# Kernel optimization log

Hardware: AMD Instinct MI355X
Metric: run time of the kernel (lower is better)

## Reference

```python
import jax, jax.numpy as jnp
import numpy as np

DIM = 1024
NUM_HEADS = 16
HEAD_DIM = DIM // NUM_HEADS
ROPE_THETA = 10000.0
SCALE = HEAD_DIM ** -0.5


def _apply_rope(x, cos, sin):
    # x: [B, H, S, head_dim]; cos/sin: [S, head_dim//2] (broadcast over B, H)
    x_even = x[..., 0::2]
    x_odd = x[..., 1::2]
    rot_even = x_even * cos - x_odd * sin
    rot_odd = x_even * sin + x_odd * cos
    # interleave back: stack on last axis then flatten, matching torch .stack(-1).flatten(-2)
    return jnp.stack([rot_even, rot_odd], axis=-1).reshape(x.shape)


def setup_inputs() -> dict:
    key = jax.random.key(0)
    k0, k1, k2 = jax.random.split(key, 3)
    B, S = 2, 2048
    x = jax.random.normal(k0, (B, S, DIM), dtype=jnp.float32)
    # small_init: std = sqrt(2 / (5*dim))
    qkv_w = jax.random.normal(k1, (3 * DIM, DIM), dtype=jnp.float32) * (2.0 / (5 * DIM)) ** 0.5
    qkv_b = jnp.zeros((3 * DIM,), dtype=jnp.float32)
    # wang_init: std = 2 / num_blocks / sqrt(dim) scaled
    out_w = jax.random.normal(k2, (DIM, DIM), dtype=jnp.float32) * (2.0 / DIM) ** 0.5 / 2.0
    out_b = jnp.zeros((DIM,), dtype=jnp.float32)
    return {"x": x, "qkv_w": qkv_w, "qkv_b": qkv_b, "out_w": out_w, "out_b": out_b, "window_size": 512}


def reference(x, qkv_w, qkv_b, out_w, out_b, window_size):
    B, S, D = x.shape
    qkv = x @ qkv_w.T + qkv_b                          # [B, S, 3D]
    qkv = qkv.reshape(B, S, 3, NUM_HEADS, HEAD_DIM).transpose(2, 0, 3, 1, 4)
    q, k, v = qkv[0], qkv[1], qkv[2]                   # each [B, H, S, hd]

    pos = jnp.arange(S, dtype=jnp.float32)
    inv_freq = 1.0 / (ROPE_THETA ** (jnp.arange(0, HEAD_DIM, 2, dtype=jnp.float32) / HEAD_DIM))
    freqs = pos[:, None] * inv_freq                    # [S, hd//2]
    cos, sin = jnp.cos(freqs), jnp.sin(freqs)
    q = _apply_rope(q, cos, sin)
    k = _apply_rope(k, cos, sin)

    scores = jnp.einsum('bhqd,bhkd->bhqk', q, k) * SCALE
    i = jnp.arange(S)
    mask = (i[:, None] >= i[None, :]) & ((i[:, None] - i[None, :]) < window_size)  # causal sliding window
    scores = jnp.where(mask, scores, -jnp.inf)
    attn = jax.nn.softmax(scores, axis=-1)
    out = jnp.einsum('bhqk,bhkd->bhqd', attn, v)       # [B, H, S, hd]
    out = out.transpose(0, 2, 1, 3).reshape(B, S, D)
    return out @ out_w.T + out_b
```

## Files before the change

kernel.cpp:

```cpp
#include <hip/hip_runtime.h>
#include <hip/hip_bf16.h>
#include <cstdint>
#include <cstddef>

using bf16x8 = __attribute__((ext_vector_type(8))) short;
using f32x4  = __attribute__((ext_vector_type(4))) float;

#define MFMA16(a, b, c) __builtin_amdgcn_mfma_f32_16x16x32_bf16((a), (b), (c), 0, 0, 0)

__device__ __forceinline__ unsigned short f2bf(float f) {
    unsigned int u = __float_as_uint(f);
    u += 0x7fffu + ((u >> 16) & 1u);
    return (unsigned short)(u >> 16);
}
__device__ __forceinline__ uint32_t pack2bf(float a, float b) {
    __hip_bfloat162 h = __float22bfloat162_rn(float2{a, b});
    return *(uint32_t*)&h;
}
__device__ __forceinline__ float bflo(uint32_t p) { return __uint_as_float(p << 16); }
__device__ __forceinline__ float bfhi(uint32_t p) { return __uint_as_float(p & 0xffff0000u); }

__device__ __forceinline__ void gload_lds16(const void* g, void* l) {
    __builtin_amdgcn_global_load_lds(
        (const __attribute__((address_space(1))) void*)g,
        (__attribute__((address_space(3))) void*)l, 16, 0, 0);
}

#define S_LEN 2048
#define NHEAD 16
#define HDIM  64
#define DIM   1024
#define WIN   512
#define BATCH 2
#define MROWS 4096

__global__ void prep(float* __restrict__ cosT, float* __restrict__ sinT,
                     const float* __restrict__ x, unsigned short* __restrict__ xb,
                     const float* __restrict__ qw, unsigned short* __restrict__ qwb,
                     const float* __restrict__ ow, unsigned short* __restrict__ owb) {
    int t = blockIdx.x * 256 + threadIdx.x;
    if (t < 65536) {
        int s = t >> 5, f = t & 31;
        float invf = powf(10000.0f, -(float)f / 32.0f);
        float ang = (float)s * invf;
        cosT[t] = cosf(ang);
        sinT[t] = sinf(ang);
        return;
    }
    int u = t - 65536;
    const float* src;
    unsigned short* dst;
    int i;
    if (u < 1048576)        { src = x;  dst = xb;  i = u * 4; }
    else if (u < 1835008)   { src = qw; dst = qwb; i = (u - 1048576) * 4; }
    else                    { src = ow; dst = owb; i = (u - 1835008) * 4; }
    float4 v = *(const float4*)(src + i);
    ushort4 o;
    o.x = f2bf(v.x); o.y = f2bf(v.y); o.z = f2bf(v.z); o.w = f2bf(v.w);
    *(ushort4*)(dst + i) = o;
}

template <int OUT_BF16>
__global__ __launch_bounds__(256) void gemm_nt(const unsigned short* __restrict__ A,
                                               const unsigned short* __restrict__ Bw,
                                               const float* __restrict__ bias,
                                               void* __restrict__ Cout, int N, int K) {
    __shared__ short As[128 * 32];
    __shared__ short Bs[128 * 32];
    const int tid = threadIdx.x;
    const int lane = tid & 63, w = tid >> 6;
    const int wr = w >> 1, wc = w & 1, lm = lane & 15, lg = lane >> 4;
    const int row0 = blockIdx.y * 128, col0 = blockIdx.x * 128;

    f32x4 acc[4][4];
#pragma unroll
    for (int m = 0; m < 4; ++m)
#pragma unroll
        for (int n = 0; n < 4; ++n) acc[m][n] = (f32x4){0.f, 0.f, 0.f, 0.f};

    const size_t ldb = (size_t)K * 2;
    for (int kt = 0; kt < K; kt += 32) {
#pragma unroll
        for (int i = 0; i < 2; ++i) {
            int c = tid + 256 * i;
            int r = c >> 2, kc = c & 3;
            gload_lds16((const char*)A  + (size_t)(row0 + r) * ldb + (size_t)kt * 2 + kc * 16, &As[c * 8]);
            gload_lds16((const char*)Bw + (size_t)(col0 + r) * ldb + (size_t)kt * 2 + kc * 16, &Bs[c * 8]);
        }
        __syncthreads();
        bf16x8 af[4], bfr[4];
#pragma unroll
        for (int m = 0; m < 4; ++m) af[m]  = *(const bf16x8*)&As[(wr * 64 + m * 16 + lm) * 32 + lg * 8];
#pragma unroll
        for (int n = 0; n < 4; ++n) bfr[n] = *(const bf16x8*)&Bs[(wc * 64 + n * 16 + lm) * 32 + lg * 8];
#pragma unroll
        for (int m = 0; m < 4; ++m)
#pragma unroll
            for (int n = 0; n < 4; ++n) acc[m][n] = MFMA16(af[m], bfr[n], acc[m][n]);
        __syncthreads();
    }

#pragma unroll
    for (int m = 0; m < 4; ++m) {
        int row = row0 + wr * 64 + m * 16 + lg * 4;
#pragma unroll
        for (int n = 0; n < 4; ++n) {
            int col = col0 + wc * 64 + n * 16 + lm;
            float bv = bias[col];
#pragma unroll
            for (int r = 0; r < 4; ++r) {
                float v = acc[m][n][r] + bv;
                if (OUT_BF16)
                    ((unsigned short*)Cout)[(size_t)(row + r) * N + col] = f2bf(v);
                else
                    ((float*)Cout)[(size_t)(row + r) * N + col] = v;
            }
        }
    }
}

__global__ void rope_pack(const unsigned short* __restrict__ qkvb,
                          const float* __restrict__ cosT, const float* __restrict__ sinT,
                          unsigned short* __restrict__ qb, unsigned short* __restrict__ kb) {
    int t = blockIdx.x * 256 + threadIdx.x;
    int p = t & 511, m = t >> 9;
    int h = p >> 5, f = p & 31;
    int s = m & (S_LEN - 1), b = m >> 11;
    float c = cosT[s * 32 + f], sn = sinT[s * 32 + f];
    const float SC = 0.125f;

    uint32_t qp = *(const uint32_t*)&qkvb[m * 3072 + h * 64 + 2 * f];
    float qe = bflo(qp), qo = bfhi(qp);
    float re = (qe * c - qo * sn) * SC, ro = (qe * sn + qo * c) * SC;
    *(uint32_t*)&qb[((b * NHEAD + h) * S_LEN + s) * 64 + 2 * f] =
        (uint32_t)f2bf(re) | ((uint32_t)f2bf(ro) << 16);

    uint32_t kp = *(const uint32_t*)&qkvb[m * 3072 + 1024 + h * 64 + 2 * f];
    float ke = bflo(kp), ko = bfhi(kp);
    float rke = ke * c - ko * sn, rko = ke * sn + ko * c;
    *(uint32_t*)&kb[((b * NHEAD + h) * S_LEN + s) * 64 + 2 * f] =
        (uint32_t)f2bf(rke) | ((uint32_t)f2bf(rko) << 16);
}

__global__ __launch_bounds__(256) void v_transpose(const unsigned short* __restrict__ qkvb,
                                                   unsigned short* __restrict__ vt) {
    int st = blockIdx.x, bh = blockIdx.y;
    int h = bh & 15, b = bh >> 4;
    __shared__ unsigned short tile[64][72];
    int tid = threadIdx.x;
#pragma unroll
    for (int i = 0; i < 2; ++i) {
        int c = tid + 256 * i;
        int r = c >> 3, col = (c & 7) * 8;
        int m = b * S_LEN + st * 64 + r;
        *(bf16x8*)&tile[r][col] = *(const bf16x8*)&qkvb[m * 3072 + 2048 + h * 64 + col];
    }
    __syncthreads();
#pragma unroll
    for (int i = 0; i < 2; ++i) {
        int c = tid + 256 * i;
        int d = c >> 3, scol = (c & 7) * 8;
        unsigned short tmp[8];
#pragma unroll
        for (int j = 0; j < 8; ++j) tmp[j] = tile[scol + j][d];
        *(bf16x8*)&vt[(size_t)bh * 64 * S_LEN + (size_t)d * S_LEN + st * 64 + scol] = *(bf16x8*)tmp;
    }
}

__global__ __launch_bounds__(256) void attn(const unsigned short* __restrict__ qb,
                                            const unsigned short* __restrict__ kb,
                                            const unsigned short* __restrict__ vt,
                                            unsigned short* __restrict__ ao) {
    const int p = blockIdx.x;
    const int L = (p & 7) * 128 + (p >> 3);
    const int qblk = L & 31, bh = L >> 5;
    const int b = bh >> 4, h = bh & 15;
    const int tid = threadIdx.x, w = tid >> 6, lane = tid & 63;
    const int lm = lane & 15, lg = lane >> 4;
    const unsigned short* Qb = qb + (size_t)bh * S_LEN * 64;
    const unsigned short* Kb = kb + (size_t)bh * S_LEN * 64;
    const unsigned short* Vt = vt + (size_t)bh * 64 * S_LEN;
    const int q0 = qblk * 64 + w * 16;

    __shared__ short Ks[2][64 * 64];
    __shared__ short Vs[2][64 * 64];
    __shared__ short Plds[4][16 * 64];
    short* Pw = Plds[w];

    bf16x8 aq0 = *(const bf16x8*)&Qb[(q0 + lm) * 64 + lg * 8];
    bf16x8 aq1 = *(const bf16x8*)&Qb[(q0 + lm) * 64 + lg * 8 + 32];

    f32x4 o[4];
#pragma unroll
    for (int n = 0; n < 4; ++n) o[n] = (f32x4){0.f, 0.f, 0.f, 0.f};
    float lsum = 0.f;

    const int qq = q0 + lm;
    const int t0 = qblk >= 8 ? qblk - 8 : 0;

    auto stage = [&](int kt, int buf) {
#pragma unroll
        for (int i = 0; i < 2; ++i) {
            int c = tid + 256 * i;
            int r = c >> 3, g = (c & 7) ^ (r & 7);
            gload_lds16(Kb + (size_t)(kt * 64 + r) * 64 + g * 8, &Ks[buf][c * 8]);
            gload_lds16(Vt + (size_t)r * S_LEN + kt * 64 + g * 8, &Vs[buf][c * 8]);
        }
    };

    stage(t0, 0);
    __syncthreads();
    int cur = 0;
    for (int kt = t0; kt <= qblk; ++kt) {
        if (kt < qblk) stage(kt + 1, cur ^ 1);
        const int kbase = kt * 64;
        const int sw = lm & 7;
        f32x4 sT[4];
#pragma unroll
        for (int n = 0; n < 4; ++n) {
            int rl = n * 16 + lm;
            bf16x8 bk0 = *(const bf16x8*)&Ks[cur][rl * 64 + ((lg ^ sw) << 3)];
            bf16x8 bk1 = *(const bf16x8*)&Ks[cur][rl * 64 + (((lg + 4) ^ sw) << 3)];
            f32x4 z = (f32x4){0.f, 0.f, 0.f, 0.f};
            z = MFMA16(bk0, aq0, z);
            sT[n] = MFMA16(bk1, aq1, z);
        }
#pragma unroll
        for (int n = 0; n < 4; ++n) {
            int kk0 = kbase + n * 16 + lg * 4;
#pragma unroll
            for (int r = 0; r < 4; ++r) {
                int d = qq - (kk0 + r);
                float sv = ((unsigned)d < (unsigned)WIN) ? sT[n][r] : -1e30f;
                float pv = __expf(sv);
                sT[n][r] = pv;
                lsum += pv;
            }
            uint2 pk;
            pk.x = pack2bf(sT[n][0], sT[n][1]);
            pk.y = pack2bf(sT[n][2], sT[n][3]);
            *(uint2*)&Pw[lm * 64 + ((((2 * n + (lg >> 1)) ^ sw) << 3) + ((lg & 1) << 2))] = pk;
        }
        bf16x8 ap0 = *(const bf16x8*)&Pw[lm * 64 + ((lg ^ sw) << 3)];
        bf16x8 ap1 = *(const bf16x8*)&Pw[lm * 64 + (((lg + 4) ^ sw) << 3)];
#pragma unroll
        for (int n = 0; n < 4; ++n) {
            int rl = n * 16 + lm;
            bf16x8 bv0 = *(const bf16x8*)&Vs[cur][rl * 64 + ((lg ^ sw) << 3)];
            bf16x8 bv1 = *(const bf16x8*)&Vs[cur][rl * 64 + (((lg + 4) ^ sw) << 3)];
            o[n] = MFMA16(ap0, bv0, o[n]);
            o[n] = MFMA16(ap1, bv1, o[n]);
        }
        __syncthreads();
        cur ^= 1;
    }
    lsum += __shfl_xor(lsum, 16, 64);
    lsum += __shfl_xor(lsum, 32, 64);
    float linv = 1.f / lsum;
    float lrow[4];
#pragma unroll
    for (int r = 0; r < 4; ++r) lrow[r] = __shfl(linv, lg * 4 + r, 64);
#pragma unroll
    for (int n = 0; n < 4; ++n)
#pragma unroll
        for (int r = 0; r < 4; ++r) {
            int row = b * S_LEN + q0 + lg * 4 + r;
            int col = h * 64 + n * 16 + lm;
            ao[(size_t)row * DIM + col] = f2bf(o[n][r] * lrow[r]);
        }
}

extern "C" void kernel_launch(void* const* d_in, const int* in_sizes, int n_in,
                              void* d_out, int out_size, void* d_ws, size_t ws_size,
                              hipStream_t stream) {
    const float* x      = (const float*)d_in[0];
    const float* qkv_w  = (const float*)d_in[1];
    const float* qkv_b  = (const float*)d_in[2];
    const float* out_w  = (const float*)d_in[3];
    const float* out_b  = (const float*)d_in[4];
    (void)in_sizes; (void)n_in; (void)out_size; (void)ws_size;

    char* ws = (char*)d_ws;
    float*          cosT = (float*)(ws + 0);
    float*          sinT = (float*)(ws + (256 << 10));
    unsigned short* xb   = (unsigned short*)(ws + (512 << 10));
    unsigned short* wqb  = (unsigned short*)(ws + 8912896);
    unsigned short* owb  = (unsigned short*)(ws + 15204352);
    unsigned short* qkvb = (unsigned short*)(ws + 17301504);
    unsigned short* qbuf = (unsigned short*)(ws + 42467328);
    unsigned short* kbuf = (unsigned short*)(ws + 50855936);
    unsigned short* vtb  = (unsigned short*)(ws + 59244544);
    unsigned short* aob  = (unsigned short*)(ws + 67633152);

    prep<<<8448, 256, 0, stream>>>(cosT, sinT, x, xb, qkv_w, wqb, out_w, owb);

    gemm_nt<1><<<dim3(24, 32), 256, 0, stream>>>(xb, wqb, qkv_b, qkvb, 3 * DIM, DIM);

    rope_pack<<<8192, 256, 0, stream>>>(qkvb, cosT, sinT, qbuf, kbuf);
    v_transpose<<<dim3(32, 32), 256, 0, stream>>>(qkvb, vtb);

    attn<<<1024, 256, 0, stream>>>(qbuf, kbuf, vtb, aob);

    gemm_nt<0><<<dim3(8, 32), 256, 0, stream>>>(aob, owb, out_b, d_out, DIM, DIM);
}
```

Baseline: 111.4 us.

## Fuse RoPE and V transpose into QKV GEMM epilogue, double-buffer and swizzle GEMM LDS

The QKV projection GEMM now applies bias, RoPE and Q scaling in its epilogue and writes Q/K in head-major layout and V transposed, staging tiles through LDS. This removes the rope_pack and v_transpose kernels and the intermediate qkv buffer round trip. Both GEMMs also gain double-buffered LDS staging with one barrier per k-step and an XOR swizzle on LDS columns to cut bank conflicts. The epilogue adds extra barriers and LDS traffic, and the GEMMs hardcode K=1024.

```diff
diff --git a/kernel.cpp b/kernel.cpp
--- a/kernel.cpp
+++ b/kernel.cpp
@@ -16,6 +16,9 @@
 __device__ __forceinline__ uint32_t pack2bf(float a, float b) {
     __hip_bfloat162 h = __float22bfloat162_rn(float2{a, b});
     return *(uint32_t*)&h;
+}
+__device__ __forceinline__ float bf2f(short x) {
+    return __uint_as_float(((uint32_t)(unsigned short)x) << 16);
 }
 __device__ __forceinline__ float bflo(uint32_t p) { return __uint_as_float(p << 16); }
 __device__ __forceinline__ float bfhi(uint32_t p) { return __uint_as_float(p & 0xffff0000u); }
@@ -31,7 +34,6 @@
 #define HDIM  64
 #define DIM   1024
 #define WIN   512
-#define BATCH 2
 #define MROWS 4096
 
 __global__ void prep(float* __restrict__ cosT, float* __restrict__ sinT,
@@ -60,13 +62,145 @@
     *(ushort4*)(dst + i) = o;
 }
 
-template <int OUT_BF16>
-__global__ __launch_bounds__(256) void gemm_nt(const unsigned short* __restrict__ A,
-                                               const unsigned short* __restrict__ Bw,
-                                               const float* __restrict__ bias,
-                                               void* __restrict__ Cout, int N, int K) {
-    __shared__ short As[128 * 32];
-    __shared__ short Bs[128 * 32];
+
+__global__ __launch_bounds__(256) void gemm_qkv_fused(
+        const unsigned short* __restrict__ A,
+        const unsigned short* __restrict__ Bw,
+        const float* __restrict__ bias,
+        const float* __restrict__ cosT, const float* __restrict__ sinT,
+        unsigned short* __restrict__ qbuf,
+        unsigned short* __restrict__ kbuf,
+        unsigned short* __restrict__ vtb) {
+    __shared__ __align__(16) char smem_raw[32768];
+    const int tid = threadIdx.x;
+    const int lane = tid & 63, w = tid >> 6;
+    const int wr = w >> 1, wc = w & 1, lm = lane & 15, lg = lane >> 4;
+    const int bx = blockIdx.x, by = blockIdx.y;
+    const int row0 = by * 128, col0 = bx * 128;
+    const int plane = bx >> 3;
+    const int h0 = (bx & 7) * 2;
+    const int b = by >> 4, s_base = (by & 15) * 128;
+
+    f32x4 acc[4][4];
+#pragma unroll
+    for (int m = 0; m < 4; ++m)
+#pragma unroll
+        for (int n = 0; n < 4; ++n) acc[m][n] = (f32x4){0.f, 0.f, 0.f, 0.f};
+
+    auto As = [&](int buf) { return (short*)(smem_raw + buf * 16384); };
+    auto Bs = [&](int buf) { return (short*)(smem_raw + buf * 16384 + 8192); };
+
+    const size_t ldb = 2048;
+    auto stage = [&](int kt, int buf) {
+#pragma unroll
+        for (int i = 0; i < 2; ++i) {
+            int c = tid + 256 * i;
+            int r = c >> 2, gp = c & 3;
+            int gs = gp ^ ((r >> 1) & 3);
+            gload_lds16((const char*)A  + (size_t)(row0 + r) * ldb + (size_t)kt * 64 + gs * 16, As(buf) + c * 8);
+            gload_lds16((const char*)Bw + (size_t)(col0 + r) * ldb + (size_t)kt * 64 + gs * 16, Bs(buf) + c * 8);
+        }
+    };
+
+    stage(0, 0);
+    __syncthreads();
+    int cur = 0;
+    const int swz = (lm >> 1) & 3;
+    for (int kt = 0; kt < 32; ++kt) {
+        if (kt + 1 < 32) stage(kt + 1, cur ^ 1);
+        bf16x8 af[4], bfr[4];
+        const short* as = As(cur);
+        const short* bs = Bs(cur);
+#pragma unroll
+        for (int m = 0; m < 4; ++m) af[m]  = *(const bf16x8*)&as[(wr * 64 + m * 16 + lm) * 32 + ((lg ^ swz) << 3)];
+#pragma unroll
+        for (int n = 0; n < 4; ++n) bfr[n] = *(const bf16x8*)&bs[(wc * 64 + n * 16 + lm) * 32 + ((lg ^ swz) << 3)];
+#pragma unroll
+        for (int m = 0; m < 4; ++m)
+#pragma unroll
+            for (int n = 0; n < 4; ++n) acc[m][n] = MFMA16(af[m], bfr[n], acc[m][n]);
+        __syncthreads();
+        cur ^= 1;
+    }
+
+    unsigned short (*tile)[136] = (unsigned short(*)[136])smem_raw;
+    unsigned short (*tileT)[72] = (unsigned short(*)[72])smem_raw;
+    const int lane8 = tid & 7, idx = tid >> 3;
+
+#pragma unroll 1
+    for (int half = 0; half < 2; ++half) {
+        __syncthreads();
+        if (wr == half) {
+            if (plane < 2) {
+#pragma unroll
+                for (int m = 0; m < 4; ++m)
+#pragma unroll
+                    for (int n = 0; n < 4; ++n) {
+                        int colL = wc * 64 + n * 16 + lm;
+                        float bv = bias[col0 + colL];
+#pragma unroll
+                        for (int r = 0; r < 4; ++r)
+                            tile[m * 16 + lg * 4 + r][colL] = f2bf(acc[m][n][r] + bv);
+                    }
+            } else {
+#pragma unroll
+                for (int m = 0; m < 4; ++m)
+#pragma unroll
+                    for (int n = 0; n < 4; ++n) {
+                        int colL = wc * 64 + n * 16 + lm;
+                        float bv = bias[col0 + colL];
+                        uint2 pk;
+                        pk.x = pack2bf(acc[m][n][0] + bv, acc[m][n][1] + bv);
+                        pk.y = pack2bf(acc[m][n][2] + bv, acc[m][n][3] + bv);
+                        *(uint2*)&tileT[colL][m * 16 + lg * 4] = pk;
+                    }
+            }
+        }
+        __syncthreads();
+        if (plane < 2) {
+            unsigned short* dstp = (plane == 0) ? qbuf : kbuf;
+            const float qsc = (plane == 0) ? 0.125f : 1.0f;
+            int d0 = lane8 * 8;
+#pragma unroll
+            for (int j = 0; j < 2; ++j) {
+                int srow = idx + 32 * j;
+                int s = s_base + half * 64 + srow;
+                float4 c4 = *(const float4*)&cosT[s * 32 + (d0 >> 1)];
+                float4 s4 = *(const float4*)&sinT[s * 32 + (d0 >> 1)];
+#pragma unroll
+                for (int hh = 0; hh < 2; ++hh) {
+                    bf16x8 v = *(const bf16x8*)&tile[srow][hh * 64 + d0];
+                    float e0 = bf2f(v[0]), o0 = bf2f(v[1]);
+                    float e1 = bf2f(v[2]), o1 = bf2f(v[3]);
+                    float e2 = bf2f(v[4]), o2 = bf2f(v[5]);
+                    float e3 = bf2f(v[6]), o3 = bf2f(v[7]);
+                    uint4 pk;
+                    pk.x = pack2bf((e0 * c4.x - o0 * s4.x) * qsc, (e0 * s4.x + o0 * c4.x) * qsc);
+                    pk.y = pack2bf((e1 * c4.y - o1 * s4.y) * qsc, (e1 * s4.y + o1 * c4.y) * qsc);
+                    pk.z = pack2bf((e2 * c4.z - o2 * s4.z) * qsc, (e2 * s4.z + o2 * c4.z) * qsc);
+                    pk.w = pack2bf((e3 * c4.w - o3 * s4.w) * qsc, (e3 * s4.w + o3 * c4.w) * qsc);
+                    int h = h0 + hh;
+                    *(uint4*)&dstp[(((size_t)(b * NHEAD + h)) * S_LEN + s) * 64 + d0] = pk;
+                }
+            }
+        } else {
+#pragma unroll
+            for (int rr = 0; rr < 4; ++rr) {
+                int hd = rr * 32 + idx;
+                int hh = hd >> 6, d = hd & 63, h = h0 + hh;
+                bf16x8 v = *(const bf16x8*)&tileT[hd][lane8 * 8];
+                *(bf16x8*)&vtb[((size_t)(b * NHEAD + h) * 64 + d) * S_LEN +
+                               s_base + half * 64 + lane8 * 8] = v;
+            }
+        }
+    }
+}
+
+__global__ __launch_bounds__(256) void gemm_out(const unsigned short* __restrict__ A,
+                                                const unsigned short* __restrict__ Bw,
+                                                const float* __restrict__ bias,
+                                                float* __restrict__ Cout) {
+    __shared__ __align__(16) char smem_raw[32768];
     const int tid = threadIdx.x;
     const int lane = tid & 63, w = tid >> 6;
     const int wr = w >> 1, wc = w & 1, lm = lane & 15, lg = lane >> 4;
@@ -78,26 +212,40 @@
 #pragma unroll
         for (int n = 0; n < 4; ++n) acc[m][n] = (f32x4){0.f, 0.f, 0.f, 0.f};
 
-    const size_t ldb = (size_t)K * 2;
-    for (int kt = 0; kt < K; kt += 32) {
+    auto As = [&](int buf) { return (short*)(smem_raw + buf * 16384); };
+    auto Bs = [&](int buf) { return (short*)(smem_raw + buf * 16384 + 8192); };
+
+    const size_t ldb = 2048;
+    auto stage = [&](int kt, int buf) {
 #pragma unroll
         for (int i = 0; i < 2; ++i) {
             int c = tid + 256 * i;
-            int r = c >> 2, kc = c & 3;
-            gload_lds16((const char*)A  + (size_t)(row0 + r) * ldb + (size_t)kt * 2 + kc * 16, &As[c * 8]);
-            gload_lds16((const char*)Bw + (size_t)(col0 + r) * ldb + (size_t)kt * 2 + kc * 16, &Bs[c * 8]);
-        }
-        __syncthreads();
+            int r = c >> 2, gp = c & 3;
+            int gs = gp ^ ((r >> 1) & 3);
+            gload_lds16((const char*)A  + (size_t)(row0 + r) * ldb + (size_t)kt * 64 + gs * 16, As(buf) + c * 8);
+            gload_lds16((const char*)Bw + (size_t)(col0 + r) * ldb + (size_t)kt * 64 + gs * 16, Bs(buf) + c * 8);
+        }
+    };
+
+    stage(0, 0);
+    __syncthreads();
+    int cur = 0;
+    const int swz = (lm >> 1) & 3;
+    for (int kt = 0; kt < 32; ++kt) {
+        if (kt + 1 < 32) stage(kt + 1, cur ^ 1);
         bf16x8 af[4], bfr[4];
-#pragma unroll
-        for (int m = 0; m < 4; ++m) af[m]  = *(const bf16x8*)&As[(wr * 64 + m * 16 + lm) * 32 + lg * 8];
-#pragma unroll
-        for (int n = 0; n < 4; ++n) bfr[n] = *(const bf16x8*)&Bs[(wc * 64 + n * 16 + lm) * 32 + lg * 8];
+        const short* as = As(cur);
+        const short* bs = Bs(cur);
+#pragma unroll
+        for (int m = 0; m < 4; ++m) af[m]  = *(const bf16x8*)&as[(wr * 64 + m * 16 + lm) * 32 + ((lg ^ swz) << 3)];
+#pragma unroll
+        for (int n = 0; n < 4; ++n) bfr[n] = *(const bf16x8*)&bs[(wc * 64 + n * 16 + lm) * 32 + ((lg ^ swz) << 3)];
 #pragma unroll
         for (int m = 0; m < 4; ++m)
 #pragma unroll
             for (int n = 0; n < 4; ++n) acc[m][n] = MFMA16(af[m], bfr[n], acc[m][n]);
         __syncthreads();
+        cur ^= 1;
     }
 
 #pragma unroll
@@ -108,62 +256,9 @@
             int col = col0 + wc * 64 + n * 16 + lm;
             float bv = bias[col];
 #pragma unroll
-            for (int r = 0; r < 4; ++r) {
-                float v = acc[m][n][r] + bv;
-                if (OUT_BF16)
-                    ((unsigned short*)Cout)[(size_t)(row + r) * N + col] = f2bf(v);
-                else
-                    ((float*)Cout)[(size_t)(row + r) * N + col] = v;
-            }
-        }
-    }
-}
-
-__global__ void rope_pack(const unsigned short* __restrict__ qkvb,
-                          const float* __restrict__ cosT, const float* __restrict__ sinT,
-                          unsigned short* __restrict__ qb, unsigned short* __restrict__ kb) {
-    int t = blockIdx.x * 256 + threadIdx.x;
-    int p = t & 511, m = t >> 9;
-    int h = p >> 5, f = p & 31;
-    int s = m & (S_LEN - 1), b = m >> 11;
-    float c = cosT[s * 32 + f], sn = sinT[s * 32 + f];
-    const float SC = 0.125f;
-
-    uint32_t qp = *(const uint32_t*)&qkvb[m * 3072 + h * 64 + 2 * f];
-    float qe = bflo(qp), qo = bfhi(qp);
-    float re = (qe * c - qo * sn) * SC, ro = (qe * sn + qo * c) * SC;
-    *(uint32_t*)&qb[((b * NHEAD + h) * S_LEN + s) * 64 + 2 * f] =
-        (uint32_t)f2bf(re) | ((uint32_t)f2bf(ro) << 16);
-
-    uint32_t kp = *(const uint32_t*)&qkvb[m * 3072 + 1024 + h * 64 + 2 * f];
-    float ke = bflo(kp), ko = bfhi(kp);
-    float rke = ke * c - ko * sn, rko = ke * sn + ko * c;
-    *(uint32_t*)&kb[((b * NHEAD + h) * S_LEN + s) * 64 + 2 * f] =
-        (uint32_t)f2bf(rke) | ((uint32_t)f2bf(rko) << 16);
-}
-
-__global__ __launch_bounds__(256) void v_transpose(const unsigned short* __restrict__ qkvb,
-                                                   unsigned short* __restrict__ vt) {
-    int st = blockIdx.x, bh = blockIdx.y;
-    int h = bh & 15, b = bh >> 4;
-    __shared__ unsigned short tile[64][72];
-    int tid = threadIdx.x;
-#pragma unroll
-    for (int i = 0; i < 2; ++i) {
-        int c = tid + 256 * i;
-        int r = c >> 3, col = (c & 7) * 8;
-        int m = b * S_LEN + st * 64 + r;
-        *(bf16x8*)&tile[r][col] = *(const bf16x8*)&qkvb[m * 3072 + 2048 + h * 64 + col];
-    }
-    __syncthreads();
-#pragma unroll
-    for (int i = 0; i < 2; ++i) {
-        int c = tid + 256 * i;
-        int d = c >> 3, scol = (c & 7) * 8;
-        unsigned short tmp[8];
-#pragma unroll
-        for (int j = 0; j < 8; ++j) tmp[j] = tile[scol + j][d];
-        *(bf16x8*)&vt[(size_t)bh * 64 * S_LEN + (size_t)d * S_LEN + st * 64 + scol] = *(bf16x8*)tmp;
+            for (int r = 0; r < 4; ++r)
+                Cout[(size_t)(row + r) * DIM + col] = acc[m][n][r] + bv;
+        }
     }
 }
 
@@ -282,24 +377,21 @@
 
     char* ws = (char*)d_ws;
     float*          cosT = (float*)(ws + 0);
-    float*          sinT = (float*)(ws + (256 << 10));
-    unsigned short* xb   = (unsigned short*)(ws + (512 << 10));
+    float*          sinT = (float*)(ws + 262144);
+    unsigned short* xb   = (unsigned short*)(ws + 524288);
     unsigned short* wqb  = (unsigned short*)(ws + 8912896);
     unsigned short* owb  = (unsigned short*)(ws + 15204352);
-    unsigned short* qkvb = (unsigned short*)(ws + 17301504);
-    unsigned short* qbuf = (unsigned short*)(ws + 42467328);
-    unsigned short* kbuf = (unsigned short*)(ws + 50855936);
-    unsigned short* vtb  = (unsigned short*)(ws + 59244544);
-    unsigned short* aob  = (unsigned short*)(ws + 67633152);
+    unsigned short* qbuf = (unsigned short*)(ws + 17301504);
+    unsigned short* kbuf = (unsigned short*)(ws + 25690112);
+    unsigned short* vtb  = (unsigned short*)(ws + 34078720);
+    unsigned short* aob  = (unsigned short*)(ws + 42467328);
 
     prep<<<8448, 256, 0, stream>>>(cosT, sinT, x, xb, qkv_w, wqb, out_w, owb);
 
-    gemm_nt<1><<<dim3(24, 32), 256, 0, stream>>>(xb, wqb, qkv_b, qkvb, 3 * DIM, DIM);
-
-    rope_pack<<<8192, 256, 0, stream>>>(qkvb, cosT, sinT, qbuf, kbuf);
-    v_transpose<<<dim3(32, 32), 256, 0, stream>>>(qkvb, vtb);
+    gemm_qkv_fused<<<dim3(24, 32), 256, 0, stream>>>(xb, wqb, qkv_b, cosT, sinT,
+                                                     qbuf, kbuf, vtb);
 
     attn<<<1024, 256, 0, stream>>>(qbuf, kbuf, vtb, aob);
 
-    gemm_nt<0><<<dim3(8, 32), 256, 0, stream>>>(aob, owb, out_b, d_out, DIM, DIM);
-}
+    gemm_out<<<dim3(8, 32), 256, 0, stream>>>(aob, owb, out_b, (float*)d_out);
+}
```

Result: faster. 105.0 us (-5.8%).
